# Kernel optimization log

Hardware: AMD Instinct MI355X
Metric: run time of the kernel (lower is better)

The kernel has to match this reference:

```python
import jax, jax.numpy as jnp
import numpy as np

B, S, D, H = 2, 2048, 1024, 16
DH = D // H

def setup_inputs() -> dict:
    key = jax.random.key(0)
    ks = jax.random.split(key, 9)
    s = 1.0 / np.sqrt(D)
    def lin(k):
        kw, kb = jax.random.split(k)
        W = jax.random.uniform(kw, (D, D), jnp.float32, -s, s)
        b = jax.random.uniform(kb, (D,), jnp.float32, -s, s)
        return W, b
    Wq, bq = lin(ks[0]); Wk, bk = lin(ks[1]); Wv, bv = lin(ks[2]); Wo, bo = lin(ks[3])
    x = jax.random.normal(ks[4], (B, S, D), jnp.float32)
    return {"x": x, "Wq": Wq, "bq": bq, "Wk": Wk, "bk": bk,
            "Wv": Wv, "bv": bv, "Wo": Wo, "bo": bo}

def _split_heads(t):
    # [B,S,D] -> [B,H,S,DH]
    return t.reshape(B, S, H, DH).transpose(0, 2, 1, 3)

def reference(x, Wq, bq, Wk, bk, Wv, bv, Wo, bo):
    # torch Linear: y = x @ W.T + b
    q = _split_heads(x @ Wq.T + bq)
    k = _split_heads(x @ Wk.T + bk)
    v = _split_heads(x @ Wv.T + bv)
    scores = jnp.einsum('bhqd,bhkd->bhqk', q, k) / jnp.sqrt(jnp.float32(DH))
    p = jax.nn.softmax(scores, axis=-1)  # dropout is identity in eval
    o = jnp.einsum('bhqk,bhkd->bhqd', p, v)
    o = o.transpose(0, 2, 1, 3).reshape(B, S, D)  # combine heads
    return o @ Wo.T + bo
```

## Files before the change

### kernel.cpp

```cpp
#include <hip/hip_runtime.h>


typedef __bf16 bf16;
typedef bf16 bf16x8 __attribute__((ext_vector_type(8)));
typedef bf16 bf16x4 __attribute__((ext_vector_type(4)));
typedef short s16x4 __attribute__((ext_vector_type(4)));
typedef float f32x4 __attribute__((ext_vector_type(4)));

#define MFMA32(a, b, c) __builtin_amdgcn_mfma_f32_16x16x32_bf16(a, b, c, 0, 0, 0)

#if __has_builtin(__builtin_amdgcn_mfma_f32_16x16x16bf16_1k)
#define HAVE_MFMA16 1
#define MFMA16(a, b, c) __builtin_amdgcn_mfma_f32_16x16x16bf16_1k(a, b, c, 0, 0, 0)
#else
#define HAVE_MFMA16 0
#endif

#define GLL(g, l) __builtin_amdgcn_global_load_lds(                              \
    (const __attribute__((address_space(1))) void*)(const void*)(g),             \
    (__attribute__((address_space(3))) void*)(void*)(l), 16, 0, 0)

union pk4 { bf16x4 h; s16x4 s; unsigned int d[2]; };

__global__ __launch_bounds__(256)
void cvt_bf16(const float* __restrict__ x,  const float* __restrict__ Wq,
              const float* __restrict__ Wk, const float* __restrict__ Wv,
              const float* __restrict__ Wo,
              bf16* __restrict__ xb, bf16* __restrict__ wqb, bf16* __restrict__ wkb,
              bf16* __restrict__ wvb, bf16* __restrict__ wob)
{
    const int idx = blockIdx.x * 256 + threadIdx.x;
    const float* src; bf16* dst; int off;
    if (idx < 1048576) { src = x; dst = xb; off = idx; }
    else {
        const int r = idx - 1048576;
        const int seg = r >> 18;
        off = r & 262143;
        src = (seg == 0) ? Wq : (seg == 1) ? Wk : (seg == 2) ? Wv : Wo;
        dst = (seg == 0) ? wqb : (seg == 1) ? wkb : (seg == 2) ? wvb : wob;
    }
    const float4 v = ((const float4*)src)[off];
    bf16x4 o = {(bf16)v.x, (bf16)v.y, (bf16)v.z, (bf16)v.w};
    *(bf16x4*)(dst + (size_t)off * 4) = o;
}

__global__ __launch_bounds__(256)
void qkv_gemm(const bf16* __restrict__ xb,
              const bf16* __restrict__ wqb, const float* __restrict__ bq,
              const bf16* __restrict__ wkb, const float* __restrict__ bk,
              const bf16* __restrict__ wvb, const float* __restrict__ bv,
              bf16* __restrict__ q_ws, bf16* __restrict__ k_ws, bf16* __restrict__ v_ws)
{
    const int z = blockIdx.z;
    const bf16*  W    = (z == 0) ? wqb : (z == 1) ? wkb : wvb;
    const float* bias = (z == 0) ? bq  : (z == 1) ? bk  : bv;

    __shared__ bf16 As[128][32];
    __shared__ bf16 Bs[128][32];
    __shared__ char ebuf[17408];
    bf16 (*Et)[68]  = (bf16(*)[68])ebuf;
    bf16 (*Vt)[132] = (bf16(*)[132])ebuf;

    const int m0 = blockIdx.x * 128;
    const int n0 = blockIdx.y * 128;
    const int t    = threadIdx.x;
    const int wave = t >> 6;
    const int lane = t & 63;
    const int lr   = lane & 15;
    const int quad = lane >> 4;
    const int wm = (wave & 1) * 64;
    const int wn = (wave >> 1) * 64;

    const int srow = wave * 32 + (lane >> 2);
    const int scol = (lane & 3) * 8;
    const bf16* ga0 = xb + (size_t)(m0 + srow) * 1024 + scol;
    const bf16* ga1 = xb + (size_t)(m0 + srow + 16) * 1024 + scol;
    const bf16* gb0 = W  + (size_t)(n0 + srow) * 1024 + scol;
    const bf16* gb1 = W  + (size_t)(n0 + srow + 16) * 1024 + scol;
    bf16* la0 = &As[srow][scol];
    bf16* la1 = &As[srow + 16][scol];
    bf16* lb0 = &Bs[srow][scol];
    bf16* lb1 = &Bs[srow + 16][scol];

    f32x4 acc[4][4] = {};

    for (int k0 = 0; k0 < 1024; k0 += 32) {
        GLL(ga0 + k0, la0);
        GLL(ga1 + k0, la1);
        GLL(gb0 + k0, lb0);
        GLL(gb1 + k0, lb1);
        __syncthreads();

        bf16x8 af[4], bfr[4];
        #pragma unroll
        for (int i = 0; i < 4; i++) af[i]  = *(const bf16x8*)&As[wm + i*16 + lr][quad*8];
        #pragma unroll
        for (int j = 0; j < 4; j++) bfr[j] = *(const bf16x8*)&Bs[wn + j*16 + lr][quad*8];
        #pragma unroll
        for (int i = 0; i < 4; i++)
            #pragma unroll
            for (int j = 0; j < 4; j++)
                acc[i][j] = MFMA32(af[i], bfr[j], acc[i][j]);
        __syncthreads();
    }

    const int bi = m0 >> 11, si0 = m0 & 2047;
    if (z < 2) {
        bf16* hw = (z == 0) ? q_ws : k_ws;
        const float sc = (z == 0) ? 0.125f : 1.0f;
        #pragma unroll
        for (int ph = 0; ph < 2; ph++) {
            if ((wave >> 1) == ph) {
                #pragma unroll
                for (int j = 0; j < 4; j++) {
                    const float bb = bias[n0 + ph * 64 + j * 16 + lr];
                    #pragma unroll
                    for (int i = 0; i < 4; i++)
                        #pragma unroll
                        for (int r = 0; r < 4; r++)
                            Et[wm + i*16 + quad*4 + r][j*16 + lr] =
                                (bf16)((acc[i][j][r] + bb) * sc);
                }
            }
            __syncthreads();
            const int hh = (n0 >> 6) + ph;
            bf16* dst = hw + (((size_t)bi * 16 + hh) * 2048 + si0) * 64;
            const int row = t >> 1, cc = (t & 1) * 32;
            #pragma unroll
            for (int e = 0; e < 4; e++)
                *(bf16x8*)(dst + (size_t)row * 64 + cc + e * 8) =
                    *(const bf16x8*)&Et[row][cc + e * 8];
            __syncthreads();
        }
    } else {
        #pragma unroll
        for (int ph = 0; ph < 2; ph++) {
            if ((wave >> 1) == ph) {
                #pragma unroll
                for (int j = 0; j < 4; j++) {
                    const float bb = bias[n0 + ph * 64 + j * 16 + lr];
                    #pragma unroll
                    for (int i = 0; i < 4; i++)
                        #pragma unroll
                        for (int r = 0; r < 4; r++)
                            Vt[j * 16 + lr][wm + i * 16 + quad * 4 + r] =
                                (bf16)(acc[i][j][r] + bb);
                }
            }
            __syncthreads();
            const int c  = t >> 2;
            const int sc_ = (t & 3) * 32;
            const int col = n0 + ph * 64 + c;
            const int h = col >> 6, dh = col & 63;
            bf16* dst = v_ws + (((size_t)bi * 16 + h) * 64 + dh) * 2048 + si0 + sc_;
            #pragma unroll
            for (int e = 0; e < 4; e++)
                *(bf16x8*)(dst + e * 8) = *(const bf16x8*)&Vt[c][sc_ + e * 8];
            __syncthreads();
        }
    }
}

__global__ __launch_bounds__(256, 4)
void attn(const bf16* __restrict__ q_ws, const bf16* __restrict__ k_ws,
          const bf16* __restrict__ v_ws, bf16* __restrict__ o_ws)
{
    const int qt = blockIdx.x;
    const int bh = blockIdx.y;
    const int b_ = bh >> 4, h = bh & 15;

    const bf16* qbase = q_ws + (size_t)bh * 2048 * 64;
    const bf16* kbase = k_ws + (size_t)bh * 2048 * 64;
    const bf16* vbase = v_ws + (size_t)bh * 64 * 2048;

    __shared__ bf16 Ks[128][72];
    __shared__ bf16 Vs[64][136];

    const int t    = threadIdx.x;
    const int wave = t >> 6;
    const int lane = t & 63;
    const int lr   = lane & 15;
    const int quad = lane >> 4;

    bf16x8 aq[2];
    #pragma unroll
    for (int kc = 0; kc < 2; kc++)
        aq[kc] = *(const bf16x8*)(qbase +
            (size_t)(qt*64 + wave*16 + lr) * 64 + kc*32 + quad*8);

    float m_i = -1e30f, l_i = 0.f;
    f32x4 o_accT[4] = {};
    const float C = 1.44269504f;

    bf16x8 kreg[4], vreg[4];
    #pragma unroll
    for (int u = 0; u < 4; u++) {
        const int c = t + u * 256;
        kreg[u] = *(const bf16x8*)(kbase + (size_t)c * 8);
        vreg[u] = *(const bf16x8*)(vbase + (size_t)(c >> 4) * 2048 + (c & 15) * 8);
    }

    for (int kt = 0; kt < 16; kt++) {
        __syncthreads();
        #pragma unroll
        for (int u = 0; u < 4; u++) {
            const int c = t + u * 256;
            *(bf16x8*)&Ks[c >> 3][(c & 7) * 8] = kreg[u];
            *(bf16x8*)&Vs[c >> 4][(c & 15) * 8] = vreg[u];
        }
        __syncthreads();
        if (kt < 15) {
            #pragma unroll
            for (int u = 0; u < 4; u++) {
                const int c = t + u * 256;
                kreg[u] = *(const bf16x8*)(kbase + (size_t)(kt+1) * 8192 + c * 8);
                vreg[u] = *(const bf16x8*)(vbase + (size_t)(c >> 4) * 2048
                                           + (kt+1) * 128 + (c & 15) * 8);
            }
        }

        f32x4 sacc[8];
        #pragma unroll
        for (int j = 0; j < 8; j++) {
            bf16x8 kf0 = *(const bf16x8*)&Ks[j*16 + lr][quad*8];
            bf16x8 kf1 = *(const bf16x8*)&Ks[j*16 + lr][32 + quad*8];
            f32x4 a = {0.f, 0.f, 0.f, 0.f};
            a = MFMA32(kf0, aq[0], a);
            a = MFMA32(kf1, aq[1], a);
            sacc[j] = a;
        }

        float m = -1e30f;
        #pragma unroll
        for (int j = 0; j < 8; j++)
            #pragma unroll
            for (int r = 0; r < 4; r++) m = fmaxf(m, sacc[j][r]);
        m = fmaxf(m, __shfl_xor(m, 16));
        m = fmaxf(m, __shfl_xor(m, 32));
        const float nm = fmaxf(m_i, m);
        const float al = exp2f((m_i - nm) * C);
        m_i = nm;
        const float nmc = nm * C;
        float rs = 0.f;
        #pragma unroll
        for (int j = 0; j < 8; j++)
            #pragma unroll
            for (int r = 0; r < 4; r++) {
                const float p = exp2f(fmaf(sacc[j][r], C, -nmc));
                sacc[j][r] = p;
                rs += p;
            }
        #pragma unroll
        for (int n = 0; n < 4; n++)
            #pragma unroll
            for (int r = 0; r < 4; r++) o_accT[n][r] *= al;
        rs += __shfl_xor(rs, 16);
        rs += __shfl_xor(rs, 32);
        l_i = l_i * al + rs;

#if HAVE_MFMA16
        #pragma unroll
        for (int j = 0; j < 8; j++) {
            pk4 pf;
            pf.h = bf16x4{(bf16)sacc[j][0], (bf16)sacc[j][1],
                          (bf16)sacc[j][2], (bf16)sacc[j][3]};
            #pragma unroll
            for (int fb = 0; fb < 4; fb++) {
                pk4 vf;
                *(unsigned long long*)vf.d =
                    *(const unsigned long long*)&Vs[fb*16 + lr][j*16 + quad*4];
                o_accT[fb] = MFMA16(vf.s, pf.s, o_accT[fb]);
            }
        }
#else
        unsigned int p0[8], p1[8];
        #pragma unroll
        for (int j = 0; j < 8; j++) {
            pk4 pf;
            pf.h = bf16x4{(bf16)sacc[j][0], (bf16)sacc[j][1],
                          (bf16)sacc[j][2], (bf16)sacc[j][3]};
            p0[j] = pf.d[0]; p1[j] = pf.d[1];
        }
        const int srcA = lr + 16 * ((2 * quad) & 3);
        const int srcB = lr + 16 * ((2 * quad + 1) & 3);
        const bool hi = (quad >> 1) != 0;
        #pragma unroll
        for (int c = 0; c < 4; c++) {
            unsigned int a0 = __shfl(p0[2*c], srcA), a1 = __shfl(p0[2*c+1], srcA);
            unsigned int b0 = __shfl(p1[2*c], srcA), b1 = __shfl(p1[2*c+1], srcA);
            unsigned int c0 = __shfl(p0[2*c], srcB), c1 = __shfl(p0[2*c+1], srcB);
            unsigned int d0 = __shfl(p1[2*c], srcB), d1 = __shfl(p1[2*c+1], srcB);
            unsigned int fr[4];
            fr[0] = hi ? a1 : a0;
            fr[1] = hi ? b1 : b0;
            fr[2] = hi ? c1 : c0;
            fr[3] = hi ? d1 : d0;
            bf16x8 pf8 = *(bf16x8*)fr;
            #pragma unroll
            for (int fb = 0; fb < 4; fb++) {
                bf16x8 vf8 = *(const bf16x8*)&Vs[fb*16 + lr][c*32 + quad*8];
                o_accT[fb] = MFMA32(vf8, pf8, o_accT[fb]);
            }
        }
#endif
    }

    __syncthreads();
    bf16 (*OsE)[68] = (bf16(*)[68])&Ks[0][0];
    const float inv = 1.0f / l_i;
    const int sil = wave * 16 + lr;
    #pragma unroll
    for (int fb = 0; fb < 4; fb++)
        #pragma unroll
        for (int r = 0; r < 4; r++)
            OsE[sil][fb*16 + quad*4 + r] = (bf16)(o_accT[fb][r] * inv);
    __syncthreads();
    const int row = t >> 2, seg = (t & 3) * 16;
    bf16* dst = o_ws + ((size_t)b_ * 2048 + qt*64 + row) * 1024 + h*64 + seg;
    *(bf16x8*)(dst)     = *(const bf16x8*)&OsE[row][seg];
    *(bf16x8*)(dst + 8) = *(const bf16x8*)&OsE[row][seg + 8];
}

__global__ __launch_bounds__(256)
void out_gemm(const bf16* __restrict__ o_ws,
              const bf16* __restrict__ wob, const float* __restrict__ bo,
              float* __restrict__ out)
{
    __shared__ bf16 As[64][32];
    __shared__ bf16 Bs[128][32];
    __shared__ float Ot[64][68];

    const int m0 = blockIdx.x * 64;
    const int n0 = blockIdx.y * 128;
    const int t    = threadIdx.x;
    const int wave = t >> 6;
    const int lane = t & 63;
    const int lr   = lane & 15;
    const int quad = lane >> 4;
    const int wm = (wave & 1) * 32;
    const int wn = (wave >> 1) * 64;

    const int srowA = wave * 16 + (lane >> 2);
    const int srowB = wave * 32 + (lane >> 2);
    const int scol  = (lane & 3) * 8;
    const bf16* gaA = o_ws + (size_t)(m0 + srowA) * 1024 + scol;
    const bf16* gb0 = wob  + (size_t)(n0 + srowB) * 1024 + scol;
    const bf16* gb1 = wob  + (size_t)(n0 + srowB + 16) * 1024 + scol;
    bf16* laA = &As[srowA][scol];
    bf16* lb0 = &Bs[srowB][scol];
    bf16* lb1 = &Bs[srowB + 16][scol];

    f32x4 acc[2][4] = {};

    for (int k0 = 0; k0 < 1024; k0 += 32) {
        GLL(gaA + k0, laA);
        GLL(gb0 + k0, lb0);
        GLL(gb1 + k0, lb1);
        __syncthreads();

        bf16x8 af[2], bfr[4];
        #pragma unroll
        for (int i = 0; i < 2; i++) af[i]  = *(const bf16x8*)&As[wm + i*16 + lr][quad*8];
        #pragma unroll
        for (int j = 0; j < 4; j++) bfr[j] = *(const bf16x8*)&Bs[wn + j*16 + lr][quad*8];
        #pragma unroll
        for (int i = 0; i < 2; i++)
            #pragma unroll
            for (int j = 0; j < 4; j++)
                acc[i][j] = MFMA32(af[i], bfr[j], acc[i][j]);
        __syncthreads();
    }

    #pragma unroll
    for (int ph = 0; ph < 2; ph++) {
        if ((wave >> 1) == ph) {
            #pragma unroll
            for (int j = 0; j < 4; j++) {
                const float bb = bo[n0 + ph * 64 + j * 16 + lr];
                #pragma unroll
                for (int i = 0; i < 2; i++)
                    #pragma unroll
                    for (int r = 0; r < 4; r++)
                        Ot[wm + i*16 + quad*4 + r][j*16 + lr] = acc[i][j][r] + bb;
            }
        }
        __syncthreads();
        const int row = t >> 2, seg = (t & 3) * 16;
        float* dst = out + (size_t)(m0 + row) * 1024 + n0 + ph * 64 + seg;
        #pragma unroll
        for (int e = 0; e < 4; e++)
            *(float4*)(dst + e * 4) = *(const float4*)&Ot[row][seg + e * 4];
        __syncthreads();
    }
}

extern "C" void kernel_launch(void* const* d_in, const int* in_sizes, int n_in,
                              void* d_out, int out_size, void* d_ws, size_t ws_size,
                              hipStream_t stream) {
    (void)in_sizes; (void)n_in; (void)out_size; (void)ws_size;
    const float* x  = (const float*)d_in[0];
    const float* Wq = (const float*)d_in[1];
    const float* bq = (const float*)d_in[2];
    const float* Wk = (const float*)d_in[3];
    const float* bk = (const float*)d_in[4];
    const float* Wv = (const float*)d_in[5];
    const float* bv = (const float*)d_in[6];
    const float* Wo = (const float*)d_in[7];
    const float* bo = (const float*)d_in[8];
    float* out = (float*)d_out;

    char* ws = (char*)d_ws;
    const size_t MB = 1024 * 1024;
    bf16* xb   = (bf16*)(ws);
    bf16* wqb  = (bf16*)(ws + 8 * MB);
    bf16* wkb  = (bf16*)(ws + 10 * MB);
    bf16* wvb  = (bf16*)(ws + 12 * MB);
    bf16* wob  = (bf16*)(ws + 14 * MB);
    bf16* q_ws = (bf16*)(ws + 16 * MB);
    bf16* k_ws = (bf16*)(ws + 24 * MB);
    bf16* v_ws = (bf16*)(ws + 32 * MB);
    bf16* o_ws = (bf16*)(ws + 40 * MB);

    hipLaunchKernelGGL(cvt_bf16, dim3(8192), dim3(256), 0, stream,
                       x, Wq, Wk, Wv, Wo, xb, wqb, wkb, wvb, wob);
    hipLaunchKernelGGL(qkv_gemm, dim3(32, 8, 3), dim3(256), 0, stream,
                       xb, wqb, bq, wkb, bk, wvb, bv, q_ws, k_ws, v_ws);
    hipLaunchKernelGGL(attn, dim3(32, 32), dim3(256), 0, stream,
                       q_ws, k_ws, v_ws, o_ws);
    hipLaunchKernelGGL(out_gemm, dim3(64, 8), dim3(256), 0, stream,
                       o_ws, wob, bo, out);
}
```

Measured before the change: 240.1 us.

## Double GEMM K-tile with XOR-swizzled LDS and fold softmax into PV MFMAs

Both projection GEMMs now stage 64-wide K tiles instead of 32, with an XOR swizzle applied to global source columns and to LDS reads. This halves the barrier count and avoids LDS bank conflicts, and occupancy hints of 3 blocks are added. In attention, V is repacked into LDS so each thread reads it as wide 16-byte vectors. The exp/bf16 conversion is interleaved with the PV MFMAs, and the row sum is computed with an MFMA against a ones vector instead of shuffle reductions. The trade-offs are more LDS per block and register pressure under the occupancy bound.

```diff
diff --git a/kernel.cpp b/kernel.cpp
--- a/kernel.cpp
+++ b/kernel.cpp
@@ -21,6 +21,7 @@
     (__attribute__((address_space(3))) void*)(void*)(l), 16, 0, 0)
 
 union pk4 { bf16x4 h; s16x4 s; unsigned int d[2]; };
+union v8u { bf16x8 v; bf16x4 h[2]; s16x4 s[2]; };
 
 __global__ __launch_bounds__(256)
 void cvt_bf16(const float* __restrict__ x,  const float* __restrict__ Wq,
@@ -44,7 +45,7 @@
     *(bf16x4*)(dst + (size_t)off * 4) = o;
 }
 
-__global__ __launch_bounds__(256)
+__global__ __launch_bounds__(256, 3)
 void qkv_gemm(const bf16* __restrict__ xb,
               const bf16* __restrict__ wqb, const float* __restrict__ bq,
               const bf16* __restrict__ wkb, const float* __restrict__ bk,
@@ -55,8 +56,8 @@
     const bf16*  W    = (z == 0) ? wqb : (z == 1) ? wkb : wvb;
     const float* bias = (z == 0) ? bq  : (z == 1) ? bk  : bv;
 
-    __shared__ bf16 As[128][32];
-    __shared__ bf16 Bs[128][32];
+    __shared__ bf16 As[128][64];
+    __shared__ bf16 Bs[128][64];
     __shared__ char ebuf[17408];
     bf16 (*Et)[68]  = (bf16(*)[68])ebuf;
     bf16 (*Vt)[132] = (bf16(*)[132])ebuf;
@@ -71,36 +72,48 @@
     const int wm = (wave & 1) * 64;
     const int wn = (wave >> 1) * 64;
 
-    const int srow = wave * 32 + (lane >> 2);
-    const int scol = (lane & 3) * 8;
-    const bf16* ga0 = xb + (size_t)(m0 + srow) * 1024 + scol;
-    const bf16* ga1 = xb + (size_t)(m0 + srow + 16) * 1024 + scol;
-    const bf16* gb0 = W  + (size_t)(n0 + srow) * 1024 + scol;
-    const bf16* gb1 = W  + (size_t)(n0 + srow + 16) * 1024 + scol;
-    bf16* la0 = &As[srow][scol];
-    bf16* la1 = &As[srow + 16][scol];
-    bf16* lb0 = &Bs[srow][scol];
-    bf16* lb1 = &Bs[srow + 16][scol];
+    const int srow8 = lane >> 3;
+    const int pcol  = (lane & 7) * 8;
+    const int gcol  = ((lane & 7) ^ (lane >> 3)) * 8;
+    const bf16* gaU[4]; const bf16* gbU[4]; bf16* laU[4]; bf16* lbU[4];
+    #pragma unroll
+    for (int u = 0; u < 4; u++) {
+        const int row = wave * 32 + u * 8 + srow8;
+        gaU[u] = xb + (size_t)(m0 + row) * 1024 + gcol;
+        gbU[u] = W  + (size_t)(n0 + row) * 1024 + gcol;
+        laU[u] = &As[row][pcol];
+        lbU[u] = &Bs[row][pcol];
+    }
+    const int swA = (lr & 7) * 8;
 
     f32x4 acc[4][4] = {};
 
-    for (int k0 = 0; k0 < 1024; k0 += 32) {
-        GLL(ga0 + k0, la0);
-        GLL(ga1 + k0, la1);
-        GLL(gb0 + k0, lb0);
-        GLL(gb1 + k0, lb1);
-        __syncthreads();
-
-        bf16x8 af[4], bfr[4];
-        #pragma unroll
-        for (int i = 0; i < 4; i++) af[i]  = *(const bf16x8*)&As[wm + i*16 + lr][quad*8];
-        #pragma unroll
-        for (int j = 0; j < 4; j++) bfr[j] = *(const bf16x8*)&Bs[wn + j*16 + lr][quad*8];
+    for (int k0 = 0; k0 < 1024; k0 += 64) {
+        #pragma unroll
+        for (int u = 0; u < 4; u++) {
+            GLL(gaU[u] + k0, laU[u]);
+            GLL(gbU[u] + k0, lbU[u]);
+        }
+        __syncthreads();
+
+        bf16x8 af[4][2], bfr[4][2];
         #pragma unroll
         for (int i = 0; i < 4; i++)
             #pragma unroll
-            for (int j = 0; j < 4; j++)
-                acc[i][j] = MFMA32(af[i], bfr[j], acc[i][j]);
+            for (int kc = 0; kc < 2; kc++)
+                af[i][kc] = *(const bf16x8*)&As[wm + i*16 + lr][(kc*32 + quad*8) ^ swA];
+        #pragma unroll
+        for (int j = 0; j < 4; j++)
+            #pragma unroll
+            for (int kc = 0; kc < 2; kc++)
+                bfr[j][kc] = *(const bf16x8*)&Bs[wn + j*16 + lr][(kc*32 + quad*8) ^ swA];
+        #pragma unroll
+        for (int kc = 0; kc < 2; kc++)
+            #pragma unroll
+            for (int i = 0; i < 4; i++)
+                #pragma unroll
+                for (int j = 0; j < 4; j++)
+                    acc[i][j] = MFMA32(af[i][kc], bfr[j][kc], acc[i][j]);
         __syncthreads();
     }
 
@@ -191,6 +204,7 @@
     float m_i = -1e30f, l_i = 0.f;
     f32x4 o_accT[4] = {};
     const float C = 1.44269504f;
+    const s16x4 ones = {0x3F80, 0x3F80, 0x3F80, 0x3F80};
 
     bf16x8 kreg[4], vreg[4];
     #pragma unroll
@@ -206,7 +220,15 @@
         for (int u = 0; u < 4; u++) {
             const int c = t + u * 256;
             *(bf16x8*)&Ks[c >> 3][(c & 7) * 8] = kreg[u];
+#if HAVE_MFMA16
+            const int d = c >> 4, k_ = c & 15;
+            const int lo = (k_ & 1) * 64 + (k_ >> 1) * 4;
+            v8u vv; vv.v = vreg[u];
+            *(bf16x4*)&Vs[d][lo]      = vv.h[0];
+            *(bf16x4*)&Vs[d][lo + 32] = vv.h[1];
+#else
             *(bf16x8*)&Vs[c >> 4][(c & 15) * 8] = vreg[u];
+#endif
         }
         __syncthreads();
         if (kt < 15) {
@@ -241,6 +263,36 @@
         const float al = exp2f((m_i - nm) * C);
         m_i = nm;
         const float nmc = nm * C;
+        #pragma unroll
+        for (int n = 0; n < 4; n++)
+            #pragma unroll
+            for (int r = 0; r < 4; r++) o_accT[n][r] *= al;
+
+#if HAVE_MFMA16
+        f32x4 lacc = {0.f, 0.f, 0.f, 0.f};
+        #pragma unroll
+        for (int c4 = 0; c4 < 4; c4++) {
+            v8u vf[4];
+            #pragma unroll
+            for (int fb = 0; fb < 4; fb++)
+                vf[fb].v = *(const bf16x8*)&Vs[fb*16 + lr][quad*32 + c4*8];
+            #pragma unroll
+            for (int jj = 0; jj < 2; jj++) {
+                const int j = c4*2 + jj;
+                pk4 pf;
+                pf.h = bf16x4{
+                    (bf16)exp2f(fmaf(sacc[j][0], C, -nmc)),
+                    (bf16)exp2f(fmaf(sacc[j][1], C, -nmc)),
+                    (bf16)exp2f(fmaf(sacc[j][2], C, -nmc)),
+                    (bf16)exp2f(fmaf(sacc[j][3], C, -nmc))};
+                #pragma unroll
+                for (int fb = 0; fb < 4; fb++)
+                    o_accT[fb] = MFMA16(vf[fb].s[jj], pf.s, o_accT[fb]);
+                lacc = MFMA16(ones, pf.s, lacc);
+            }
+        }
+        l_i = l_i * al + lacc[0];
+#else
         float rs = 0.f;
         #pragma unroll
         for (int j = 0; j < 8; j++)
@@ -250,29 +302,9 @@
                 sacc[j][r] = p;
                 rs += p;
             }
-        #pragma unroll
-        for (int n = 0; n < 4; n++)
-            #pragma unroll
-            for (int r = 0; r < 4; r++) o_accT[n][r] *= al;
         rs += __shfl_xor(rs, 16);
         rs += __shfl_xor(rs, 32);
         l_i = l_i * al + rs;
-
-#if HAVE_MFMA16
-        #pragma unroll
-        for (int j = 0; j < 8; j++) {
-            pk4 pf;
-            pf.h = bf16x4{(bf16)sacc[j][0], (bf16)sacc[j][1],
-                          (bf16)sacc[j][2], (bf16)sacc[j][3]};
-            #pragma unroll
-            for (int fb = 0; fb < 4; fb++) {
-                pk4 vf;
-                *(unsigned long long*)vf.d =
-                    *(const unsigned long long*)&Vs[fb*16 + lr][j*16 + quad*4];
-                o_accT[fb] = MFMA16(vf.s, pf.s, o_accT[fb]);
-            }
-        }
-#else
         unsigned int p0[8], p1[8];
         #pragma unroll
         for (int j = 0; j < 8; j++) {
@@ -321,13 +353,13 @@
     *(bf16x8*)(dst + 8) = *(const bf16x8*)&OsE[row][seg + 8];
 }
 
-__global__ __launch_bounds__(256)
+__global__ __launch_bounds__(256, 3)
 void out_gemm(const bf16* __restrict__ o_ws,
               const bf16* __restrict__ wob, const float* __restrict__ bo,
               float* __restrict__ out)
 {
-    __shared__ bf16 As[64][32];
-    __shared__ bf16 Bs[128][32];
+    __shared__ bf16 As[64][64];
+    __shared__ bf16 Bs[128][64];
     __shared__ float Ot[64][68];
 
     const int m0 = blockIdx.x * 64;
@@ -340,34 +372,52 @@
     const int wm = (wave & 1) * 32;
     const int wn = (wave >> 1) * 64;
 
-    const int srowA = wave * 16 + (lane >> 2);
-    const int srowB = wave * 32 + (lane >> 2);
-    const int scol  = (lane & 3) * 8;
-    const bf16* gaA = o_ws + (size_t)(m0 + srowA) * 1024 + scol;
-    const bf16* gb0 = wob  + (size_t)(n0 + srowB) * 1024 + scol;
-    const bf16* gb1 = wob  + (size_t)(n0 + srowB + 16) * 1024 + scol;
-    bf16* laA = &As[srowA][scol];
-    bf16* lb0 = &Bs[srowB][scol];
-    bf16* lb1 = &Bs[srowB + 16][scol];
+    const int srow8 = lane >> 3;
+    const int pcol  = (lane & 7) * 8;
+    const int gcol  = ((lane & 7) ^ (lane >> 3)) * 8;
+    const bf16* gaU[2]; bf16* laU[2];
+    #pragma unroll
+    for (int u = 0; u < 2; u++) {
+        const int row = wave * 16 + u * 8 + srow8;
+        gaU[u] = o_ws + (size_t)(m0 + row) * 1024 + gcol;
+        laU[u] = &As[row][pcol];
+    }
+    const bf16* gbU[4]; bf16* lbU[4];
+    #pragma unroll
+    for (int u = 0; u < 4; u++) {
+        const int row = wave * 32 + u * 8 + srow8;
+        gbU[u] = wob + (size_t)(n0 + row) * 1024 + gcol;
+        lbU[u] = &Bs[row][pcol];
+    }
+    const int swA = (lr & 7) * 8;
 
     f32x4 acc[2][4] = {};
 
-    for (int k0 = 0; k0 < 1024; k0 += 32) {
-        GLL(gaA + k0, laA);
-        GLL(gb0 + k0, lb0);
-        GLL(gb1 + k0, lb1);
-        __syncthreads();
-
-        bf16x8 af[2], bfr[4];
-        #pragma unroll
-        for (int i = 0; i < 2; i++) af[i]  = *(const bf16x8*)&As[wm + i*16 + lr][quad*8];
-        #pragma unroll
-        for (int j = 0; j < 4; j++) bfr[j] = *(const bf16x8*)&Bs[wn + j*16 + lr][quad*8];
+    for (int k0 = 0; k0 < 1024; k0 += 64) {
+        #pragma unroll
+        for (int u = 0; u < 2; u++) GLL(gaU[u] + k0, laU[u]);
+        #pragma unroll
+        for (int u = 0; u < 4; u++) GLL(gbU[u] + k0, lbU[u]);
+        __syncthreads();
+
+        bf16x8 af[2][2], bfr[4][2];
         #pragma unroll
         for (int i = 0; i < 2; i++)
             #pragma unroll
-            for (int j = 0; j < 4; j++)
-                acc[i][j] = MFMA32(af[i], bfr[j], acc[i][j]);
+            for (int kc = 0; kc < 2; kc++)
+                af[i][kc] = *(const bf16x8*)&As[wm + i*16 + lr][(kc*32 + quad*8) ^ swA];
+        #pragma unroll
+        for (int j = 0; j < 4; j++)
+            #pragma unroll
+            for (int kc = 0; kc < 2; kc++)
+                bfr[j][kc] = *(const bf16x8*)&Bs[wn + j*16 + lr][(kc*32 + quad*8) ^ swA];
+        #pragma unroll
+        for (int kc = 0; kc < 2; kc++)
+            #pragma unroll
+            for (int i = 0; i < 2; i++)
+                #pragma unroll
+                for (int j = 0; j < 4; j++)
+                    acc[i][j] = MFMA32(af[i][kc], bfr[j][kc], acc[i][j]);
         __syncthreads();
     }
 
```

After: 230.3 us. -4.1%, faster.
